# Performance work log

Measured on AMD Instinct MI355X. Metric: run time of the kernel, lower is better.

The kernel has to match this reference:

```python
import jax, jax.numpy as jnp
import numpy as np
import math

B, S, D_MODEL, N_HEAD, D_HEAD, D_FFN = 1, 2048, 1024, 16, 64, 4096
EPS = 1e-6


def setup_inputs() -> dict:
    key = jax.random.key(0)
    ks = jax.random.split(key, 10)
    scale = 0.02
    x = jax.random.normal(ks[0], (B, S, D_MODEL), dtype=jnp.float32)
    # RoPE frequencies: freqs_cis[s, i] = exp(1j * s * theta_i), theta_i = 10000^{-2i/d_head}
    half = D_HEAD // 2
    inv_freq = 1.0 / (10000.0 ** (jnp.arange(0, half, dtype=jnp.float32) * 2.0 / D_HEAD))
    angles = jnp.arange(S, dtype=jnp.float32)[:, None] * inv_freq[None, :]  # [S, half]
    freqs_cos = jnp.cos(angles)
    freqs_sin = jnp.sin(angles)
    wq = jax.random.normal(ks[1], (D_MODEL, N_HEAD * D_HEAD), dtype=jnp.float32) * scale
    wk = jax.random.normal(ks[2], (D_MODEL, N_HEAD * D_HEAD), dtype=jnp.float32) * scale
    wv = jax.random.normal(ks[3], (D_MODEL, N_HEAD * D_HEAD), dtype=jnp.float32) * scale
    wo = jax.random.normal(ks[4], (N_HEAD * D_HEAD, D_MODEL), dtype=jnp.float32) * scale
    w1 = jax.random.normal(ks[5], (D_MODEL, D_FFN), dtype=jnp.float32) * scale
    w2 = jax.random.normal(ks[6], (D_FFN, D_MODEL), dtype=jnp.float32) * scale
    w3 = jax.random.normal(ks[7], (D_MODEL, D_FFN), dtype=jnp.float32) * scale
    attn_norm_w = jnp.ones((D_MODEL,), dtype=jnp.float32)
    ffn_norm_w = jnp.ones((D_MODEL,), dtype=jnp.float32)
    return {"x": x, "freqs_cos": freqs_cos, "freqs_sin": freqs_sin,
            "wq": wq, "wk": wk, "wv": wv, "wo": wo,
            "w1": w1, "w2": w2, "w3": w3,
            "attn_norm_w": attn_norm_w, "ffn_norm_w": ffn_norm_w}


def _rmsnorm(x, w):
    xf = x.astype(jnp.float32)
    inv = jax.lax.rsqrt(jnp.mean(xf * xf, axis=-1, keepdims=True) + EPS)
    return (xf * inv).astype(x.dtype) * w


def _rope(t, cos, sin):
    # t: [B, S, H, D]; treat last dim as interleaved (even, odd) complex pairs
    b, s, h, d = t.shape
    tr = t.astype(jnp.float32).reshape(b, s, h, d // 2, 2)
    te, to = tr[..., 0], tr[..., 1]
    c = cos[None, :, None, :]
    sn = sin[None, :, None, :]
    out = jnp.stack([te * c - to * sn, te * sn + to * c], axis=-1)
    return out.reshape(b, s, h, d).astype(t.dtype)


def reference(x, freqs_cos, freqs_sin, wq, wk, wv, wo, w1, w2, w3, attn_norm_w, ffn_norm_w):
    bsz, seqlen, _ = x.shape
    # --- attention sub-block ---
    hin = _rmsnorm(x, attn_norm_w)
    q = (hin @ wq).reshape(bsz, seqlen, N_HEAD, D_HEAD)
    k = (hin @ wk).reshape(bsz, seqlen, N_HEAD, D_HEAD)
    v = (hin @ wv).reshape(bsz, seqlen, N_HEAD, D_HEAD)
    q = _rope(q, freqs_cos, freqs_sin)
    k = _rope(k, freqs_cos, freqs_sin)
    # [B, H, S, S] scores, softmax in fp32 (no causal mask in original)
    scores = jnp.einsum('bqhd,bkhd->bhqk', q, k) / math.sqrt(D_HEAD)
    probs = jax.nn.softmax(scores.astype(jnp.float32), axis=-1).astype(q.dtype)
    attn = jnp.einsum('bhqk,bkhd->bqhd', probs, v).reshape(bsz, seqlen, N_HEAD * D_HEAD)
    h = x + attn @ wo
    # --- SwiGLU FFN sub-block ---
    f = _rmsnorm(h, ffn_norm_w)
    ffn = (jax.nn.silu(f @ w1) * (f @ w3)) @ w2
    return h + ffn
```

## Files before the change

kernel.cpp:

```cpp
#include <hip/hip_runtime.h>
#include <stdint.h>
#include <stddef.h>

using bf16x8 = __attribute__((ext_vector_type(8))) __bf16;
using f32x4  = __attribute__((ext_vector_type(4))) float;
using f32x16 = __attribute__((ext_vector_type(16))) float;

__device__ __forceinline__ float bf2f(unsigned short u) {
  union { unsigned int i; float f; } v; v.i = ((unsigned int)u) << 16; return v.f;
}
__device__ __forceinline__ unsigned short f2bf(float f) {
  union { float f; unsigned int i; } v; v.f = f;
  unsigned int r = v.i + 0x7fffu + ((v.i >> 16) & 1u);
  return (unsigned short)(r >> 16);
}
__device__ __forceinline__ unsigned short f2bf_trunc(float f) {
  union { float f; unsigned int i; } v; v.f = f;
  return (unsigned short)(v.i >> 16);
}
__device__ __forceinline__ void async16(const void* g, void* l) {
  __builtin_amdgcn_global_load_lds(
      (const __attribute__((address_space(1))) unsigned int*)g,
      (__attribute__((address_space(3))) unsigned int*)l, 16, 0, 0);
}

#define S_LEN 2048
#define DMODEL 1024
#define NHEAD 16
#define DHEAD 64
#define DFFN 4096

struct TAll {
  const float *wq, *wk, *wv, *wo, *w1, *w3, *w2;
  unsigned short *qkvT, *woT, *w13I, *w2T;
};
__global__ __launch_bounds__(256) void transpose_all_k(TAll j) {
  __shared__ unsigned short tile[32][33];
  const int tx = threadIdx.x & 31;
  const int ty = threadIdx.x >> 5;
  const unsigned u = blockIdx.x;

  const float* in;
  unsigned short* out;
  int bc, br, inC, outR, rs, rb;
  if (u < 4096) {
    int z = u >> 10;
    bc = (u & 31) * 32; br = ((u >> 5) & 31) * 32;
    in = z == 0 ? j.wq : z == 1 ? j.wk : z == 2 ? j.wv : j.wo;
    out = z == 3 ? j.woT : j.qkvT + (size_t)z * 1048576;
    inC = 1024; outR = 1024; rs = 32; rb = 0;
  } else if (u < 12288) {
    unsigned v = u - 4096;
    int z = v >> 12;
    bc = (v & 127) * 32; br = ((v >> 7) & 31) * 32;
    in = z ? j.w3 : j.w1;
    out = j.w13I;
    inC = 4096; outR = 1024; rs = 64; rb = z * 32;
  } else {
    unsigned v = u - 12288;
    bc = (v & 31) * 32; br = (v >> 5) * 32;
    in = j.w2; out = j.w2T;
    inC = 1024; outR = 4096; rs = 32; rb = 0;
  }
#pragma unroll
  for (int i = 0; i < 4; ++i)
    tile[ty + i * 8][tx] = f2bf(in[(size_t)(br + ty + i * 8) * inC + bc + tx]);
  __syncthreads();
#pragma unroll
  for (int i = 0; i < 4; ++i) {
    int c = bc + ty + i * 8;
    int dest = (c >> 5) * rs + rb + (c & 31);
    out[(size_t)dest * outR + br + tx] = tile[tx][ty + i * 8];
  }
}

__global__ __launch_bounds__(256) void vtrans_k(
    const unsigned short* __restrict__ QKV, unsigned short* __restrict__ VtG) {
  __shared__ unsigned short tile[32][33];
  const int tx = threadIdx.x & 31;
  const int ty = threadIdx.x >> 5;
  const int bc = blockIdx.x * 32;
  const int br = blockIdx.y * 32;
#pragma unroll
  for (int i = 0; i < 4; ++i)
    tile[ty + i * 8][tx] = QKV[(size_t)(br + ty + i * 8) * 3072 + 2048 + bc + tx];
  __syncthreads();
#pragma unroll
  for (int i = 0; i < 4; ++i)
    VtG[(size_t)(bc + ty + i * 8) * 2048 + br + tx] = tile[tx][ty + i * 8];
}

__global__ __launch_bounds__(256) void rmsnorm_k(
    const float* __restrict__ X, const float* __restrict__ W,
    unsigned short* __restrict__ Y) {
  const int row = blockIdx.x;
  const int t = threadIdx.x;
  const int lane = t & 63, w = t >> 6;
  const float* x = X + (size_t)row * DMODEL;
  float xs[4];
  float s = 0.f;
#pragma unroll
  for (int i = 0; i < 4; ++i) {
    xs[i] = x[t * 4 + i];
    s += xs[i] * xs[i];
  }
#pragma unroll
  for (int m = 1; m < 64; m <<= 1) s += __shfl_xor(s, m, 64);
  __shared__ float red[4];
  if (lane == 0) red[w] = s;
  __syncthreads();
  float tot = red[0] + red[1] + red[2] + red[3];
  float inv = rsqrtf(tot * (1.0f / DMODEL) + 1e-6f);
#pragma unroll
  for (int i = 0; i < 4; ++i)
    Y[(size_t)row * DMODEL + t * 4 + i] = f2bf(xs[i] * inv * W[t * 4 + i]);
}

__global__ __launch_bounds__(256) void fused_res_norm_k(
    const float* __restrict__ P0, const float* __restrict__ P1,
    const float* __restrict__ R, const float* __restrict__ W,
    float* __restrict__ Hres, unsigned short* __restrict__ Hin) {
  const int row = blockIdx.x;
  const int t = threadIdx.x;
  const int lane = t & 63, w = t >> 6;
  const size_t base = (size_t)row * DMODEL;
  float hs[4];
  float s = 0.f;
#pragma unroll
  for (int i = 0; i < 4; ++i) {
    int c = t * 4 + i;
    float h = P0[base + c] + P1[base + c] + R[base + c];
    hs[i] = h;
    Hres[base + c] = h;
    s += h * h;
  }
#pragma unroll
  for (int m = 1; m < 64; m <<= 1) s += __shfl_xor(s, m, 64);
  __shared__ float red[4];
  if (lane == 0) red[w] = s;
  __syncthreads();
  float tot = red[0] + red[1] + red[2] + red[3];
  float inv = rsqrtf(tot * (1.0f / DMODEL) + 1e-6f);
#pragma unroll
  for (int i = 0; i < 4; ++i)
    Hin[base + t * 4 + i] = f2bf(hs[i] * inv * W[t * 4 + i]);
}

__global__ __launch_bounds__(256) void gemm_qkv_rope_k(
    const unsigned short* __restrict__ A,
    const unsigned short* __restrict__ BT,
    unsigned short* __restrict__ C,
    const float* __restrict__ cosp, const float* __restrict__ sinp) {
  __shared__ unsigned short As[128 * 64];
  __shared__ unsigned short Bs[128 * 64];
  const int t = threadIdx.x;
  const int lane = t & 63;
  const int w = t >> 6;
  const int qr = (w >> 1) * 64, qc = (w & 1) * 64;
  const int l31 = lane & 31, half = lane >> 5;
  const int m0 = blockIdx.y * 128, n0 = blockIdx.x * 128;
  const int K = 1024, N = 3072;

  f32x16 acc[2][2] = {};

  for (int k0 = 0; k0 < K; k0 += 64) {
    __syncthreads();
#pragma unroll
    for (int p = 0; p < 4; ++p) {
      int off = p * 2048 + t * 8;
      int r = off >> 6;
      int sc = (((off >> 3) & 7) ^ (r & 7)) * 8;
      async16(A + (size_t)(m0 + r) * K + (k0 + sc), &As[off]);
      async16(BT + (size_t)(n0 + r) * K + (k0 + sc), &Bs[off]);
    }
    __syncthreads();
#pragma unroll
    for (int ks = 0; ks < 4; ++ks) {
      const int ch = ((ks * 2 + half) ^ (l31 & 7)) * 8;
      bf16x8 a0 = *(const bf16x8*)&As[(qr + l31) * 64 + ch];
      bf16x8 a1 = *(const bf16x8*)&As[(qr + 32 + l31) * 64 + ch];
      bf16x8 b0 = *(const bf16x8*)&Bs[(qc + l31) * 64 + ch];
      bf16x8 b1 = *(const bf16x8*)&Bs[(qc + 32 + l31) * 64 + ch];
      acc[0][0] = __builtin_amdgcn_mfma_f32_32x32x16_bf16(a0, b0, acc[0][0], 0, 0, 0);
      acc[0][1] = __builtin_amdgcn_mfma_f32_32x32x16_bf16(a0, b1, acc[0][1], 0, 0, 0);
      acc[1][0] = __builtin_amdgcn_mfma_f32_32x32x16_bf16(a1, b0, acc[1][0], 0, 0, 0);
      acc[1][1] = __builtin_amdgcn_mfma_f32_32x32x16_bf16(a1, b1, acc[1][1], 0, 0, 0);
    }
  }

#pragma unroll
  for (int rt = 0; rt < 2; ++rt)
#pragma unroll
    for (int ct = 0; ct < 2; ++ct) {
      const int colbase = n0 + qc + ct * 32;
      const int cc = colbase + l31;
      if (colbase < 2048) {
        const float scale = colbase < 1024 ? 1.0f : 0.125f;
        const int i = (cc & 63) >> 1;
#pragma unroll
        for (int reg = 0; reg < 16; ++reg) {
          int rr = m0 + qr + rt * 32 + (reg & 3) + 8 * (reg >> 2) + 4 * half;
          float v = acc[rt][ct][reg];
          float vp = __shfl_xor(v, 1, 64);
          float c = cosp[rr * 32 + i];
          float sn = sinp[rr * 32 + i];
          float outv = (l31 & 1) ? (vp * sn + v * c) : (v * c - vp * sn);
          C[(size_t)rr * N + cc] = f2bf(outv * scale);
        }
      } else {
#pragma unroll
        for (int reg = 0; reg < 16; ++reg) {
          int rr = m0 + qr + rt * 32 + (reg & 3) + 8 * (reg >> 2) + 4 * half;
          C[(size_t)rr * N + cc] = f2bf(acc[rt][ct][reg]);
        }
      }
    }
}

__global__ __launch_bounds__(256) void gemm_gated_k(
    const unsigned short* __restrict__ A,
    const unsigned short* __restrict__ BT,
    unsigned short* __restrict__ C) {
  __shared__ unsigned short As[256 * 64];
  __shared__ unsigned short Bs[128 * 64];
  const int t = threadIdx.x;
  const int lane = t & 63;
  const int w = t >> 6;
  const int wm = w >> 1, wn = w & 1;
  const int l31 = lane & 31, half = lane >> 5;
  const int m0 = blockIdx.y * 256, n0 = blockIdx.x * 128;
  const int K = 1024;

  f32x16 acc[4][2] = {};

  for (int k0 = 0; k0 < K; k0 += 64) {
    __syncthreads();
#pragma unroll
    for (int p = 0; p < 8; ++p) {
      int off = p * 2048 + t * 8;
      int r = off >> 6;
      int sc = (((off >> 3) & 7) ^ (r & 7)) * 8;
      async16(A + (size_t)(m0 + r) * K + (k0 + sc), &As[off]);
    }
#pragma unroll
    for (int p = 0; p < 4; ++p) {
      int off = p * 2048 + t * 8;
      int r = off >> 6;
      int sc = (((off >> 3) & 7) ^ (r & 7)) * 8;
      async16(BT + (size_t)(n0 + r) * K + (k0 + sc), &Bs[off]);
    }
    __syncthreads();
#pragma unroll
    for (int ks = 0; ks < 4; ++ks) {
      const int ch = ((ks * 2 + half) ^ (l31 & 7)) * 8;
      bf16x8 b0 = *(const bf16x8*)&Bs[(wn * 64 + l31) * 64 + ch];
      bf16x8 b1 = *(const bf16x8*)&Bs[(wn * 64 + 32 + l31) * 64 + ch];
#pragma unroll
      for (int mt = 0; mt < 4; ++mt) {
        bf16x8 a = *(const bf16x8*)&As[(wm * 128 + mt * 32 + l31) * 64 + ch];
        acc[mt][0] = __builtin_amdgcn_mfma_f32_32x32x16_bf16(a, b0, acc[mt][0], 0, 0, 0);
        acc[mt][1] = __builtin_amdgcn_mfma_f32_32x32x16_bf16(a, b1, acc[mt][1], 0, 0, 0);
      }
    }
  }

  const int cc = ((n0 + wn * 64) >> 1) + l31;
#pragma unroll
  for (int mt = 0; mt < 4; ++mt)
#pragma unroll
    for (int reg = 0; reg < 16; ++reg) {
      int rr = m0 + wm * 128 + mt * 32 + (reg & 3) + 8 * (reg >> 2) + 4 * half;
      float g1 = acc[mt][0][reg];
      float g3 = acc[mt][1][reg];
      float f = g1 / (1.f + __expf(-g1)) * g3;
      C[(size_t)rr * 4096 + cc] = f2bf(f);
    }
}

struct PtrPair { float* p0; float* p1; };

__global__ __launch_bounds__(256) void gemm_bt_sk(
    const unsigned short* __restrict__ A, int lda,
    const unsigned short* __restrict__ BT,
    PtrPair parts, int Kc, int Ktot, int N) {
  __shared__ unsigned short As[64 * 64];
  __shared__ unsigned short Bs[128 * 64];
  const int t = threadIdx.x;
  const int lane = t & 63;
  const int w = t >> 6;
  const int qr = (w >> 1) * 32, qc = (w & 1) * 64;
  const int l31 = lane & 31, half = lane >> 5;
  const int m0 = blockIdx.y * 64, n0 = blockIdx.x * 128;
  const int kb = blockIdx.z * Kc;

  f32x16 acc[2] = {};

  for (int k0 = 0; k0 < Kc; k0 += 64) {
    __syncthreads();
#pragma unroll
    for (int p = 0; p < 2; ++p) {
      int off = p * 2048 + t * 8;
      int r = off >> 6;
      int sc = (((off >> 3) & 7) ^ (r & 7)) * 8;
      async16(A + (size_t)(m0 + r) * lda + (kb + k0 + sc), &As[off]);
    }
#pragma unroll
    for (int p = 0; p < 4; ++p) {
      int off = p * 2048 + t * 8;
      int r = off >> 6;
      int sc = (((off >> 3) & 7) ^ (r & 7)) * 8;
      async16(BT + (size_t)(n0 + r) * Ktot + (kb + k0 + sc), &Bs[off]);
    }
    __syncthreads();
#pragma unroll
    for (int ks = 0; ks < 4; ++ks) {
      const int ch = ((ks * 2 + half) ^ (l31 & 7)) * 8;
      bf16x8 a0 = *(const bf16x8*)&As[(qr + l31) * 64 + ch];
      bf16x8 b0 = *(const bf16x8*)&Bs[(qc + l31) * 64 + ch];
      bf16x8 b1 = *(const bf16x8*)&Bs[(qc + 32 + l31) * 64 + ch];
      acc[0] = __builtin_amdgcn_mfma_f32_32x32x16_bf16(a0, b0, acc[0], 0, 0, 0);
      acc[1] = __builtin_amdgcn_mfma_f32_32x32x16_bf16(a0, b1, acc[1], 0, 0, 0);
    }
  }

  float* C = blockIdx.z ? parts.p1 : parts.p0;
#pragma unroll
  for (int ct = 0; ct < 2; ++ct)
#pragma unroll
    for (int reg = 0; reg < 16; ++reg) {
      int rr = m0 + qr + (reg & 3) + 8 * (reg >> 2) + 4 * half;
      int cc = n0 + qc + ct * 32 + l31;
      C[(size_t)rr * N + cc] = acc[ct][reg];
    }
}

__global__ __launch_bounds__(256) void reduce2_k(
    const float4* __restrict__ P0, const float4* __restrict__ P1,
    const float4* __restrict__ R, float4* __restrict__ Out, int nvec) {
  int i = blockIdx.x * 256 + threadIdx.x;
  if (i >= nvec) return;
  float4 a = P0[i], b = P1[i], r = R[i];
  float4 o;
  o.x = a.x + b.x + r.x;
  o.y = a.y + b.y + r.y;
  o.z = a.z + b.z + r.z;
  o.w = a.w + b.w + r.w;
  Out[i] = o;
}

#define VPAD 132
__device__ __forceinline__ int swz(int row, int col) { return col ^ ((row & 7) * 8); }

__global__ __launch_bounds__(256) void attn_k(
    const unsigned short* __restrict__ QKV,
    const unsigned short* __restrict__ VtG,
    float* __restrict__ O0, float* __restrict__ O1,
    float* __restrict__ L) {
  const int h = blockIdx.y;
  const int qb = blockIdx.x;
  const int z = blockIdx.z;
  const int t = threadIdx.x;
  const int lane = t & 63;
  const int w = t >> 6;
  const int row16 = lane & 15, quad = lane >> 4;
  const int q0 = qb * 64 + w * 16;
  const int kbase = z * 1024;

  __shared__ unsigned short Ks[128 * 64];
  __shared__ unsigned short Vt[64 * 128];
  __shared__ unsigned short Ps[4][16 * VPAD];

  const unsigned short* Qp = QKV;
  const unsigned short* Kp = QKV + 1024;
  const unsigned short* Vg = VtG + (size_t)h * 64 * 2048;

  bf16x8 aq[2];
#pragma unroll
  for (int kk = 0; kk < 2; ++kk)
    aq[kk] = *(const bf16x8*)(Qp + (size_t)(q0 + row16) * 3072 + h * 64 + kk * 32 + quad * 8);

  f32x4 o[4] = {};
  float l_r[4] = {0.f, 0.f, 0.f, 0.f};

  bf16x8 kreg[4], vreg[4];
#pragma unroll
  for (int p = 0; p < 4; ++p) {
    int off = p * 2048 + t * 8;
    int r = off >> 6, c = off & 63;
    kreg[p] = *(const bf16x8*)(Kp + (size_t)(kbase + r) * 3072 + h * 64 + c);
    int d = off >> 7, key = off & 127;
    vreg[p] = *(const bf16x8*)(Vg + (size_t)d * 2048 + kbase + key);
  }

  for (int kb = kbase; kb < kbase + 1024; kb += 128) {
    __syncthreads();
#pragma unroll
    for (int p = 0; p < 4; ++p) {
      int off = p * 2048 + t * 8;
      int r = off >> 6, c = off & 63;
      *(bf16x8*)&Ks[r * 64 + swz(r, c)] = kreg[p];
      int d = off >> 7, key = off & 127;
      *(bf16x8*)&Vt[d * 128 + swz(d, key)] = vreg[p];
    }
    __syncthreads();
    if (kb + 128 < kbase + 1024) {
      int kb2 = kb + 128;
#pragma unroll
      for (int p = 0; p < 4; ++p) {
        int off = p * 2048 + t * 8;
        int r = off >> 6, c = off & 63;
        kreg[p] = *(const bf16x8*)(Kp + (size_t)(kb2 + r) * 3072 + h * 64 + c);
        int d = off >> 7, key = off & 127;
        vreg[p] = *(const bf16x8*)(Vg + (size_t)d * 2048 + kb2 + key);
      }
    }

    f32x4 sc[8];
#pragma unroll
    for (int tj = 0; tj < 8; ++tj) {
      int kr = tj * 16 + row16;
      bf16x8 b0 = *(const bf16x8*)&Ks[kr * 64 + swz(kr, quad * 8)];
      bf16x8 b1 = *(const bf16x8*)&Ks[kr * 64 + swz(kr, 32 + quad * 8)];
      f32x4 z4 = {};
      z4 = __builtin_amdgcn_mfma_f32_16x16x32_bf16(aq[0], b0, z4, 0, 0, 0);
      z4 = __builtin_amdgcn_mfma_f32_16x16x32_bf16(aq[1], b1, z4, 0, 0, 0);
      sc[tj] = z4;
    }

#pragma unroll
    for (int reg = 0; reg < 4; ++reg) {
      float ssum = 0.f;
#pragma unroll
      for (int tj = 0; tj < 8; ++tj) {
        float p = __expf(sc[tj][reg]);
        sc[tj][reg] = p;
        ssum += p;
      }
#pragma unroll
      for (int m = 1; m < 16; m <<= 1) ssum += __shfl_xor(ssum, m, 16);
      l_r[reg] += ssum;
    }

#pragma unroll
    for (int tj = 0; tj < 8; ++tj)
#pragma unroll
      for (int reg = 0; reg < 4; ++reg)
        Ps[w][(quad * 4 + reg) * VPAD + tj * 16 + row16] = f2bf_trunc(sc[tj][reg]);

    bf16x8 ap[4];
#pragma unroll
    for (int kk = 0; kk < 4; ++kk)
      ap[kk] = *(const bf16x8*)&Ps[w][row16 * VPAD + kk * 32 + quad * 8];
#pragma unroll
    for (int dt = 0; dt < 4; ++dt) {
      int dr = dt * 16 + row16;
#pragma unroll
      for (int kk = 0; kk < 4; ++kk) {
        bf16x8 bv = *(const bf16x8*)&Vt[dr * 128 + swz(dr, kk * 32 + quad * 8)];
        o[dt] = __builtin_amdgcn_mfma_f32_16x16x32_bf16(ap[kk], bv, o[dt], 0, 0, 0);
      }
    }
  }

  float* Op = z ? O1 : O0;
#pragma unroll
  for (int dt = 0; dt < 4; ++dt)
#pragma unroll
    for (int reg = 0; reg < 4; ++reg)
      Op[(size_t)(q0 + quad * 4 + reg) * DMODEL + h * 64 + dt * 16 + row16] = o[dt][reg];
  if (row16 == 0)
#pragma unroll
    for (int reg = 0; reg < 4; ++reg)
      L[(size_t)(h * 2 + z) * S_LEN + q0 + quad * 4 + reg] = l_r[reg];
}

__global__ __launch_bounds__(256) void attn_combine_k(
    const float4* __restrict__ O0, const float4* __restrict__ O1,
    const float* __restrict__ L, unsigned short* __restrict__ Attn) {
  int i = blockIdx.x * 256 + threadIdx.x;
  int e0 = i * 4;
  int s = e0 >> 10;
  int c = e0 & 1023;
  int h = c >> 6;
  float la = L[(size_t)(h * 2) * S_LEN + s];
  float lb = L[(size_t)(h * 2 + 1) * S_LEN + s];
  float inv = 1.f / (la + lb);
  float4 a = O0[i], b = O1[i];
  ushort4 r;
  r.x = f2bf((a.x + b.x) * inv);
  r.y = f2bf((a.y + b.y) * inv);
  r.z = f2bf((a.z + b.z) * inv);
  r.w = f2bf((a.w + b.w) * inv);
  *(ushort4*)(Attn + e0) = r;
}

extern "C" void kernel_launch(void* const* d_in, const int* in_sizes, int n_in,
                              void* d_out, int out_size, void* d_ws, size_t ws_size,
                              hipStream_t stream) {
  (void)in_sizes; (void)n_in; (void)out_size; (void)ws_size;
  const float* x    = (const float*)d_in[0];
  const float* fcos = (const float*)d_in[1];
  const float* fsin = (const float*)d_in[2];
  const float* wq   = (const float*)d_in[3];
  const float* wk   = (const float*)d_in[4];
  const float* wv   = (const float*)d_in[5];
  const float* wo   = (const float*)d_in[6];
  const float* w1   = (const float*)d_in[7];
  const float* w2   = (const float*)d_in[8];
  const float* w3   = (const float*)d_in[9];
  const float* anw  = (const float*)d_in[10];
  const float* fnw  = (const float*)d_in[11];
  float* out = (float*)d_out;
  char* ws = (char*)d_ws;

  unsigned short* WqkvT = (unsigned short*)(ws + 0);
  unsigned short* VtG   = (unsigned short*)(ws + 0);
  float*          Lbuf  = (float*)(ws + 4194304);
  unsigned short* WoT   = (unsigned short*)(ws + 6291456);
  unsigned short* QKV   = (unsigned short*)(ws + 8388608);
  unsigned short* Attn  = (unsigned short*)(ws + 20971520);
  float* Oa             = (float*)(ws + 25165824);
  float* Ob             = (float*)(ws + 37748736);
  float* P0a            = (float*)(ws + 8388608);
  float* P1a            = (float*)(ws + 25165824);
  unsigned short* F     = (unsigned short*)(ws + 0);
  float* P0b            = (float*)(ws + 16777216);
  float* P1b            = (float*)(ws + 25165824);
  unsigned short* Hin   = (unsigned short*)(ws + 33554432);
  float*          Hres  = (float*)        (ws + 37748736);
  unsigned short* W13I  = (unsigned short*)(ws + 46137344);
  unsigned short* W2T   = (unsigned short*)(ws + 62914560);

  transpose_all_k<<<16384, 256, 0, stream>>>(
      TAll{wq, wk, wv, wo, w1, w3, w2, WqkvT, WoT, W13I, W2T});

  rmsnorm_k<<<2048, 256, 0, stream>>>(x, anw, Hin);
  gemm_qkv_rope_k<<<dim3(24, 16), 256, 0, stream>>>(Hin, WqkvT, QKV, fcos, fsin);
  vtrans_k<<<dim3(32, 64), 256, 0, stream>>>(QKV, VtG);
  attn_k<<<dim3(32, 16, 2), 256, 0, stream>>>(QKV, VtG, Oa, Ob, Lbuf);
  attn_combine_k<<<2048, 256, 0, stream>>>((const float4*)Oa, (const float4*)Ob, Lbuf, Attn);
  gemm_bt_sk<<<dim3(8, 32, 2), 256, 0, stream>>>(Attn, 1024, WoT, PtrPair{P0a, P1a}, 512, 1024, 1024);
  fused_res_norm_k<<<2048, 256, 0, stream>>>(P0a, P1a, x, fnw, Hres, Hin);

  gemm_gated_k<<<dim3(64, 8), 256, 0, stream>>>(Hin, W13I, F);
  gemm_bt_sk<<<dim3(8, 32, 2), 256, 0, stream>>>(F, 4096, W2T, PtrPair{P0b, P1b}, 2048, 4096, 1024);
  reduce2_k<<<2048, 256, 0, stream>>>((const float4*)P0b, (const float4*)P1b,
                                      (const float4*)Hres, (float4*)out, 524288);
}
```

Measured before the change: 316.2 us.

## Double-buffer gated FFN GEMM and enlarge N tile to 256

Reworks the fused SiLU-gated W1/W3 GEMM to use a 256x256 output tile with a 32-wide K step and two LDS buffers. The next K slice is prefetched while MFMAs run on the current one, which removes one barrier per iteration and improves operand reuse per loaded byte. The grid drops from 512 to 256 blocks. That is close to one wave on the device, so occupancy falls, and doubling the accumulator count raises register pressure.

```diff
diff --git a/kernel.cpp b/kernel.cpp
--- a/kernel.cpp
+++ b/kernel.cpp
@@ -221,60 +221,78 @@
     const unsigned short* __restrict__ A,
     const unsigned short* __restrict__ BT,
     unsigned short* __restrict__ C) {
-  __shared__ unsigned short As[256 * 64];
-  __shared__ unsigned short Bs[128 * 64];
+  __shared__ unsigned short As[2][256 * 32];
+  __shared__ unsigned short Bs[2][256 * 32];
   const int t = threadIdx.x;
   const int lane = t & 63;
   const int w = t >> 6;
   const int wm = w >> 1, wn = w & 1;
   const int l31 = lane & 31, half = lane >> 5;
-  const int m0 = blockIdx.y * 256, n0 = blockIdx.x * 128;
+  const int m0 = blockIdx.y * 256, n0 = blockIdx.x * 256;
   const int K = 1024;
 
-  f32x16 acc[4][2] = {};
-
-  for (int k0 = 0; k0 < K; k0 += 64) {
-    __syncthreads();
-#pragma unroll
-    for (int p = 0; p < 8; ++p) {
-      int off = p * 2048 + t * 8;
-      int r = off >> 6;
-      int sc = (((off >> 3) & 7) ^ (r & 7)) * 8;
-      async16(A + (size_t)(m0 + r) * K + (k0 + sc), &As[off]);
-    }
-#pragma unroll
-    for (int p = 0; p < 4; ++p) {
-      int off = p * 2048 + t * 8;
-      int r = off >> 6;
-      int sc = (((off >> 3) & 7) ^ (r & 7)) * 8;
-      async16(BT + (size_t)(n0 + r) * K + (k0 + sc), &Bs[off]);
-    }
-    __syncthreads();
-#pragma unroll
-    for (int ks = 0; ks < 4; ++ks) {
-      const int ch = ((ks * 2 + half) ^ (l31 & 7)) * 8;
-      bf16x8 b0 = *(const bf16x8*)&Bs[(wn * 64 + l31) * 64 + ch];
-      bf16x8 b1 = *(const bf16x8*)&Bs[(wn * 64 + 32 + l31) * 64 + ch];
-#pragma unroll
-      for (int mt = 0; mt < 4; ++mt) {
-        bf16x8 a = *(const bf16x8*)&As[(wm * 128 + mt * 32 + l31) * 64 + ch];
-        acc[mt][0] = __builtin_amdgcn_mfma_f32_32x32x16_bf16(a, b0, acc[mt][0], 0, 0, 0);
-        acc[mt][1] = __builtin_amdgcn_mfma_f32_32x32x16_bf16(a, b1, acc[mt][1], 0, 0, 0);
+  f32x16 acc[4][4] = {};
+
+  int srow[4], scol[4];
+#pragma unroll
+  for (int p = 0; p < 4; ++p) {
+    int off = p * 2048 + t * 8;
+    int r = off >> 5;
+    srow[p] = r;
+    scol[p] = (((off >> 3) & 3) ^ (r & 3)) * 8;
+  }
+
+#pragma unroll
+  for (int p = 0; p < 4; ++p) {
+    int off = p * 2048 + t * 8;
+    async16(A + (size_t)(m0 + srow[p]) * K + scol[p], &As[0][off]);
+    async16(BT + (size_t)(n0 + srow[p]) * K + scol[p], &Bs[0][off]);
+  }
+
+  int cur = 0;
+  for (int k0 = 0; k0 < K; k0 += 32, cur ^= 1) {
+    __syncthreads();
+    if (k0 + 32 < K) {
+      int nk = k0 + 32;
+#pragma unroll
+      for (int p = 0; p < 4; ++p) {
+        int off = p * 2048 + t * 8;
+        async16(A + (size_t)(m0 + srow[p]) * K + (nk + scol[p]), &As[cur ^ 1][off]);
+        async16(BT + (size_t)(n0 + srow[p]) * K + (nk + scol[p]), &Bs[cur ^ 1][off]);
       }
     }
-  }
-
-  const int cc = ((n0 + wn * 64) >> 1) + l31;
+#pragma unroll
+    for (int ks = 0; ks < 2; ++ks) {
+      const int ch = ((ks * 2 + half) ^ (l31 & 3)) * 8;
+      bf16x8 a[4], b[4];
+#pragma unroll
+      for (int mt = 0; mt < 4; ++mt)
+        a[mt] = *(const bf16x8*)&As[cur][(wm * 128 + mt * 32 + l31) * 32 + ch];
+#pragma unroll
+      for (int nt = 0; nt < 4; ++nt)
+        b[nt] = *(const bf16x8*)&Bs[cur][(wn * 128 + nt * 32 + l31) * 32 + ch];
+#pragma unroll
+      for (int mt = 0; mt < 4; ++mt)
+#pragma unroll
+        for (int nt = 0; nt < 4; ++nt)
+          acc[mt][nt] = __builtin_amdgcn_mfma_f32_32x32x16_bf16(a[mt], b[nt], acc[mt][nt], 0, 0, 0);
+    }
+  }
+
+  const int ccbase = (n0 + wn * 128) >> 1;
 #pragma unroll
   for (int mt = 0; mt < 4; ++mt)
 #pragma unroll
-    for (int reg = 0; reg < 16; ++reg) {
-      int rr = m0 + wm * 128 + mt * 32 + (reg & 3) + 8 * (reg >> 2) + 4 * half;
-      float g1 = acc[mt][0][reg];
-      float g3 = acc[mt][1][reg];
-      float f = g1 / (1.f + __expf(-g1)) * g3;
-      C[(size_t)rr * 4096 + cc] = f2bf(f);
-    }
+    for (int j = 0; j < 2; ++j)
+#pragma unroll
+      for (int reg = 0; reg < 16; ++reg) {
+        int rr = m0 + wm * 128 + mt * 32 + (reg & 3) + 8 * (reg >> 2) + 4 * half;
+        int cc = ccbase + j * 32 + l31;
+        float g1 = acc[mt][2 * j][reg];
+        float g3 = acc[mt][2 * j + 1][reg];
+        float f = g1 / (1.f + __expf(-g1)) * g3;
+        C[(size_t)rr * 4096 + cc] = f2bf(f);
+      }
 }
 
 struct PtrPair { float* p0; float* p1; };
@@ -542,7 +560,7 @@
   gemm_bt_sk<<<dim3(8, 32, 2), 256, 0, stream>>>(Attn, 1024, WoT, PtrPair{P0a, P1a}, 512, 1024, 1024);
   fused_res_norm_k<<<2048, 256, 0, stream>>>(P0a, P1a, x, fnw, Hres, Hin);
 
-  gemm_gated_k<<<dim3(64, 8), 256, 0, stream>>>(Hin, W13I, F);
+  gemm_gated_k<<<dim3(32, 8), 256, 0, stream>>>(Hin, W13I, F);
   gemm_bt_sk<<<dim3(8, 32, 2), 256, 0, stream>>>(F, 4096, W2T, PtrPair{P0b, P1b}, 2048, 4096, 1024);
   reduce2_k<<<2048, 256, 0, stream>>>((const float4*)P0b, (const float4*)P1b,
                                       (const float4*)Hres, (float4*)out, 524288);
```

Measured after the change: 360.1 us. +13.9%, slower.
